# Kernel tuning notes

Hardware: AMD Instinct MI355X
Metric: run time of the kernel (lower is better)

## Reference

```python
import jax, jax.numpy as jnp
import numpy as np

DIM = 256
DEPTH = 6
HEADS = 8
DH = DIM // HEADS            # 32
BUCKET = 64
TEMP = 0.75                  # sort-net softmax temperature
FF = 4 * DIM
B, T = 4, 8192


def layernorm(x, g, b, eps=1e-5):
    m = x.mean(-1, keepdims=True)
    v = ((x - m) ** 2).mean(-1, keepdims=True)
    return (x - m) * jax.lax.rsqrt(v + eps) * g + b


def sinkhorn_attn(q, k, v):
    # q,k,v: (bh, t, dh). Bucketed attention with differentiable top-1 bucket routing
    bh, t, dh = q.shape
    nb = t // BUCKET
    bq = q.reshape(bh, nb, BUCKET, dh)
    bk = k.reshape(bh, nb, BUCKET, dh)
    bv = v.reshape(bh, nb, BUCKET, dh)
    # sort net: bucket summaries -> routing matrix R (differentiable_topk, k=1)
    sq = bq.mean(2)                                   # (bh, nb, dh)
    sk = bk.mean(2)
    R = jnp.einsum('bie,bje->bij', sq, sk) * (dh ** -0.5)
    probs = jax.nn.softmax(R / TEMP, axis=-1)
    top = jnp.max(probs, axis=-1, keepdims=True)      # (bh, nb, 1)
    idx = jnp.argmax(probs, axis=-1)                  # (bh, nb)
    Rtop = jax.nn.one_hot(idx, nb, dtype=q.dtype) * top
    # gather routed key/value buckets (weighted by routing prob)
    bk_r = jnp.einsum('bij,bjtd->bitd', Rtop, bk)
    bv_r = jnp.einsum('bij,bjtd->bitd', Rtop, bv)
    K = jnp.concatenate([bk_r, bk], axis=2)           # (bh, nb, 2*BUCKET, dh)
    V = jnp.concatenate([bv_r, bv], axis=2)
    dots = jnp.einsum('buie,buje->buij', bq, K) * (dh ** -0.5)
    attn = jax.nn.softmax(dots, axis=-1)
    out = jnp.einsum('buij,buje->buie', attn, V)
    return out.reshape(bh, t, dh)


def setup_inputs() -> dict:
    key = jax.random.key(0)
    ks = jax.random.split(key, 18)
    s = 0.02
    f32 = jnp.float32
    inp = {
        'x': jax.random.normal(ks[0], (B, DIM, T), f32),
        'pe0': jax.random.normal(ks[1], (T // BUCKET, DIM), f32) * s,
        'pe1': jax.random.normal(ks[2], (BUCKET, DIM), f32) * s,
        'ln1_g': jnp.ones((DEPTH, DIM), f32),
        'ln1_b': jnp.zeros((DEPTH, DIM), f32),
        'Wq': jax.random.normal(ks[3], (DEPTH, DIM, DIM), f32) * s,
        'Wkv': jax.random.normal(ks[4], (DEPTH, DIM, 2 * DIM), f32) * s,
        'Wo': jax.random.normal(ks[5], (DEPTH, DIM, DIM), f32) * s,
        'bo': jnp.zeros((DEPTH, DIM), f32),
        'ln2_g': jnp.ones((DEPTH, DIM), f32),
        'ln2_b': jnp.zeros((DEPTH, DIM), f32),
        'W1': jax.random.normal(ks[6], (DEPTH, DIM, FF), f32) * s,
        'b1': jnp.zeros((DEPTH, FF), f32),
        'W2': jax.random.normal(ks[7], (DEPTH, FF, DIM), f32) * s,
        'b2': jnp.zeros((DEPTH, DIM), f32),
        'gf': jnp.ones((DIM,), f32),
        'bf': jnp.zeros((DIM,), f32),
    }
    return inp


def _forward(x, pe0, pe1, ln1_g, ln1_b, Wq, Wkv, Wo, bo, ln2_g, ln2_b, W1, b1, W2, b2, gf, bf):
    b, _, t = x.shape
    y = jnp.transpose(x, (0, 2, 1))                      # (b, t, dim)
    pos = (pe0[:, None, :] + pe1[None, :, :]).reshape(-1, DIM)[:t]
    y = y + pos

    def split_heads(u):
        return u.reshape(b, t, HEADS, DH).transpose(0, 2, 1, 3).reshape(b * HEADS, t, DH)

    def step(y, p):
        g1, b1_, wq, wkv, wo, bo_, g2, b2_, w1, bb1, w2, bb2 = p
        h = layernorm(y, g1, b1_)
        q = h @ wq
        k, v = jnp.split(h @ wkv, 2, axis=-1)
        o = sinkhorn_attn(split_heads(q), split_heads(k), split_heads(v))
        o = o.reshape(b, HEADS, t, DH).transpose(0, 2, 1, 3).reshape(b, t, DIM)
        y = y + o @ wo + bo_
        h = layernorm(y, g2, b2_)
        y = y + jax.nn.gelu(h @ w1 + bb1, approximate=False) @ w2 + bb2
        return y, None

    y, _ = jax.lax.scan(step, y, (ln1_g, ln1_b, Wq, Wkv, Wo, bo, ln2_g, ln2_b, W1, b1, W2, b2))
    y = layernorm(y, gf, bf)
    return jnp.transpose(y, (0, 2, 1))


def reference(x, pe0, pe1, ln1_g, ln1_b, Wq, Wkv, Wo, bo, ln2_g, ln2_b, W1, b1, W2, b2, gf, bf):
    return _forward(x, pe0, pe1, ln1_g, ln1_b, Wq, Wkv, Wo, bo, ln2_g, ln2_b, W1, b1, W2, b2, gf, bf)
```

## Files before the change

### kernel.cpp

```cpp
#include <hip/hip_runtime.h>
#include <cstdint>
#include <cstddef>

#define T_LEN 8192
#define DIMC  256
#define NBUCK 128
#define BHEAD 32
#define MROWS 32768

typedef __attribute__((ext_vector_type(8))) short bf16x8;
typedef __attribute__((ext_vector_type(4))) float f32x4;

__device__ __forceinline__ ushort f2bf(float x) {
  union { float f; unsigned u; } v; v.f = x;
  unsigned r = v.u + 0x7fffu + ((v.u >> 16) & 1u);
  return (ushort)(r >> 16);
}
__device__ __forceinline__ float bf2f(ushort u) {
  union { unsigned u; float f; } v; v.u = ((unsigned)u) << 16; return v.f;
}

__device__ __forceinline__ void gld16(const void* g, void* l) {
  __builtin_amdgcn_global_load_lds((const __attribute__((address_space(1))) void*)g,
                                   (__attribute__((address_space(3))) void*)l, 16, 0, 0);
}

__device__ __forceinline__ float fast_gelu(float v) {
  float t2 = fmaf(v * v, 0.07135481283f, 1.5957691216f);
  float z  = v * t2;
  float e  = __expf(-z);
  return v * __builtin_amdgcn_rcpf(1.0f + e);
}

__global__ __launch_bounds__(256)
void add_pos_k(const float* __restrict__ x, const float* __restrict__ pe0,
               const float* __restrict__ pe1, float* __restrict__ y) {
  __shared__ float tile[32][33];
  int b  = blockIdx.z;
  int t0 = blockIdx.x * 32;
  int d0 = blockIdx.y * 32;
  int tj = threadIdx.x;
  int di = threadIdx.y;
#pragma unroll
  for (int k = 0; k < 4; k++) {
    int d = d0 + di + k * 8;
    tile[di + k * 8][tj] = x[((size_t)b * DIMC + d) * T_LEN + t0 + tj];
  }
  __syncthreads();
#pragma unroll
  for (int k = 0; k < 4; k++) {
    int t = t0 + di + k * 8;
    int d = d0 + tj;
    y[((size_t)b * T_LEN + t) * DIMC + d] =
        tile[tj][di + k * 8] + pe0[(size_t)(t >> 6) * DIMC + d] + pe1[(size_t)(t & 63) * DIMC + d];
  }
}

__global__ __launch_bounds__(256)
void layernorm_k(const float* __restrict__ x, const float* __restrict__ g,
                 const float* __restrict__ b, ushort* __restrict__ o) {
  int row  = blockIdx.x * 4 + (threadIdx.x >> 6);
  int lane = threadIdx.x & 63;
  const float4* xr = (const float4*)(x + (size_t)row * DIMC);
  float4 v = xr[lane];
  float s  = v.x + v.y + v.z + v.w;
  float s2 = v.x * v.x + v.y * v.y + v.z * v.z + v.w * v.w;
#pragma unroll
  for (int off = 32; off; off >>= 1) {
    s  += __shfl_xor(s, off);
    s2 += __shfl_xor(s2, off);
  }
  float mean = s * (1.0f / 256.0f);
  float var  = s2 * (1.0f / 256.0f) - mean * mean;
  float r    = rsqrtf(var + 1e-5f);
  float4 gv = ((const float4*)g)[lane];
  float4 bv = ((const float4*)b)[lane];
  ushort4 o4;
  o4.x = f2bf((v.x - mean) * r * gv.x + bv.x);
  o4.y = f2bf((v.y - mean) * r * gv.y + bv.y);
  o4.z = f2bf((v.z - mean) * r * gv.z + bv.z);
  o4.w = f2bf((v.w - mean) * r * gv.w + bv.w);
  ((ushort4*)(o + (size_t)row * DIMC))[lane] = o4;
}

__global__ __launch_bounds__(256)
void wt_bf16_k(const float* __restrict__ W, ushort* __restrict__ Wt,
               int K, int N, size_t outStride) {
  __shared__ float t[32][33];
  int l = blockIdx.z;
  const float* Wl = W + (size_t)l * K * N;
  ushort* Wtl = Wt + (size_t)l * outStride;
  int n0 = blockIdx.x * 32, k0 = blockIdx.y * 32;
  int tx = threadIdx.x, ty = threadIdx.y;
#pragma unroll
  for (int p = 0; p < 4; p++)
    t[ty + p * 8][tx] = Wl[(size_t)(k0 + ty + p * 8) * N + n0 + tx];
  __syncthreads();
#pragma unroll
  for (int p = 0; p < 4; p++)
    Wtl[(size_t)(n0 + ty + p * 8) * K + k0 + tx] = f2bf(t[tx][ty + p * 8]);
}

template <int EPI>
__global__ __launch_bounds__(256)
void gemm_bf16(const ushort* __restrict__ A, const ushort* __restrict__ Bt,
               const float* __restrict__ bias, ushort* __restrict__ Cbf,
               int N, int K, int lda, int ldb) {
  __shared__ ushort sm[2][8192];
  int tid = threadIdx.x;
  int w = tid >> 6, lane = tid & 63;
  int bm = blockIdx.x << 7, bn = blockIdx.y << 7;
  int wm = (w >> 1) << 6, wn = (w & 1) << 6;
  int l15 = lane & 15, quad = lane >> 4;

  int off0 = (w << 11) + (lane << 4);
  int r0 = off0 >> 6;
  int r1 = (off0 + 1024) >> 6;
  int swc = (((lane & 3) ^ ((lane >> 3) & 3)) << 3);
  const ushort* ga0 = A + (size_t)(bm + r0) * lda + swc;
  const ushort* ga1 = A + (size_t)(bm + r1) * lda + swc;
  const ushort* gb0 = Bt + (size_t)(bn + r0) * ldb + swc;
  const ushort* gb1 = Bt + (size_t)(bn + r1) * ldb + swc;
  int aoff0 = (w << 10);
  int aoff1 = aoff0 + 512;
  int boff0 = 4096 + (w << 10);
  int boff1 = boff0 + 512;

  int sq = quad ^ ((l15 >> 1) & 3);

  f32x4 acc[4][4];
#pragma unroll
  for (int i = 0; i < 4; i++)
#pragma unroll
    for (int j = 0; j < 4; j++) {
      f32x4 z = {0.f, 0.f, 0.f, 0.f};
      acc[i][j] = z;
    }

  gld16(ga0, &sm[0][aoff0]);
  gld16(ga1, &sm[0][aoff1]);
  gld16(gb0, &sm[0][boff0]);
  gld16(gb1, &sm[0][boff1]);
  __syncthreads();

  int cur = 0;
  for (int k0 = 0; k0 < K; k0 += 32) {
    if (k0 + 32 < K) {
      ushort* S = sm[cur ^ 1];
      gld16(ga0 + k0 + 32, S + aoff0);
      gld16(ga1 + k0 + 32, S + aoff1);
      gld16(gb0 + k0 + 32, S + boff0);
      gld16(gb1 + k0 + 32, S + boff1);
    }
    const ushort* Sc = sm[cur];
    bf16x8 aF[4], bF[4];
#pragma unroll
    for (int i = 0; i < 4; i++)
      aF[i] = *(const bf16x8*)(Sc + ((wm + (i << 4) + l15) << 5) + (sq << 3));
#pragma unroll
    for (int j = 0; j < 4; j++)
      bF[j] = *(const bf16x8*)(Sc + 4096 + ((wn + (j << 4) + l15) << 5) + (sq << 3));
#pragma unroll
    for (int i = 0; i < 4; i++)
#pragma unroll
      for (int j = 0; j < 4; j++)
        acc[i][j] = __builtin_amdgcn_mfma_f32_16x16x32_bf16(aF[i], bF[j], acc[i][j], 0, 0, 0);
    __syncthreads();
    cur ^= 1;
  }

  ushort (*eb)[16][66] = (ushort(*)[16][66])&sm[0][0];
  float bvj[4];
  if (EPI == 1) {
#pragma unroll
    for (int j = 0; j < 4; j++) bvj[j] = bias[bn + wn + (j << 4) + l15];
  }
#pragma unroll
  for (int i = 0; i < 4; i++) {
#pragma unroll
    for (int j = 0; j < 4; j++) {
#pragma unroll
      for (int r = 0; r < 4; r++) {
        float v = acc[i][j][r];
        if (EPI == 1) v = fast_gelu(v + bvj[j]);
        eb[w][(quad << 2) + r][(j << 4) + l15] = f2bf(v);
      }
    }
#pragma unroll
    for (int h = 0; h < 2; h++) {
      int chunk = (h << 6) + lane;
      int row = chunk >> 3, c8 = (chunk & 7) << 3;
      bf16x8 vv = *(const bf16x8*)&eb[w][row][c8];
      *(bf16x8*)&Cbf[(size_t)(bm + wm + (i << 4) + row) * N + bn + wn + c8] = vv;
    }
  }
}

template <int FINAL>
__global__ __launch_bounds__(512)
void oproj_ln_k(const ushort* __restrict__ A, const ushort* __restrict__ Bt,
                const float* __restrict__ bias, float* __restrict__ y,
                const float* __restrict__ g, const float* __restrict__ b,
                ushort* __restrict__ obf, int K, int lda) {
  __shared__ ushort smem[20480];
  int tid = threadIdx.x;
  int wid = tid >> 6, lane = tid & 63;
  int l15 = lane & 15, quad = lane >> 4;
  int bm = blockIdx.x << 6;
  int wm = (wid >> 2) << 5;
  int wn = (wid & 3) << 6;

  const ushort* gaB[2]; int lBoff[2];
#pragma unroll
  for (int p = 0; p < 2; p++) {
    int u = tid + (p << 9);
    int row = u >> 2, ch = u & 3;
    gaB[p] = Bt + (size_t)row * K + ((ch ^ ((row >> 1) & 3)) << 3);
    lBoff[p] = 2048 + (u << 3);
  }
  bool doA = (tid < 256);
  const ushort* gaA = A + (size_t)(bm + (tid >> 2)) * lda +
                      (((tid & 3) ^ ((tid >> 3) & 3)) << 3);
  int lAoff = tid << 3;

  int sq = quad ^ ((l15 >> 1) & 3);

  f32x4 acc[2][4];
#pragma unroll
  for (int i = 0; i < 2; i++)
#pragma unroll
    for (int j = 0; j < 4; j++) {
      f32x4 z = {0.f, 0.f, 0.f, 0.f};
      acc[i][j] = z;
    }

  if (doA) gld16(gaA, smem + lAoff);
#pragma unroll
  for (int p = 0; p < 2; p++) gld16(gaB[p], smem + lBoff[p]);
  __syncthreads();

  int cur = 0;
  for (int k0 = 0; k0 < K; k0 += 32) {
    if (k0 + 32 < K) {
      ushort* S = smem + ((cur ^ 1) ? 10240 : 0);
      if (doA) gld16(gaA + k0 + 32, S + lAoff);
#pragma unroll
      for (int p = 0; p < 2; p++) gld16(gaB[p] + k0 + 32, S + lBoff[p]);
    }
    const ushort* Sc = smem + (cur ? 10240 : 0);
    bf16x8 aF[2], bF[4];
#pragma unroll
    for (int i = 0; i < 2; i++)
      aF[i] = *(const bf16x8*)(Sc + ((wm + (i << 4) + l15) << 5) + (sq << 3));
#pragma unroll
    for (int j = 0; j < 4; j++)
      bF[j] = *(const bf16x8*)(Sc + 2048 + ((wn + (j << 4) + l15) << 5) + (sq << 3));
#pragma unroll
    for (int i = 0; i < 2; i++)
#pragma unroll
      for (int j = 0; j < 4; j++)
        acc[i][j] = __builtin_amdgcn_mfma_f32_16x16x32_bf16(aF[i], bF[j], acc[i][j], 0, 0, 0);
    __syncthreads();
    cur ^= 1;
  }

  float* vbuf = (float*)smem;
  float4 b4  = ((const float4*)bias)[lane];
  float4 g4  = ((const float4*)g)[lane];
  float4 bb4 = ((const float4*)b)[lane];
#pragma unroll
  for (int h = 0; h < 2; h++) {
    if ((wid >> 2) == h) {
#pragma unroll
      for (int i = 0; i < 2; i++)
#pragma unroll
        for (int j = 0; j < 4; j++)
#pragma unroll
          for (int r = 0; r < 4; r++)
            vbuf[((i << 4) + (quad << 2) + r) * 260 + wn + (j << 4) + l15] = acc[i][j][r];
    }
    __syncthreads();
#pragma unroll
    for (int rr = 0; rr < 4; rr++) {
      int lrow = (wid << 2) + rr;
      int row = bm + (h << 5) + lrow;
      float4 a4 = *(const float4*)&vbuf[lrow * 260 + (lane << 2)];
      const float4* yrow = (const float4*)&y[(size_t)row * 256];
      float4 y4 = yrow[lane];
      float4 v4;
      v4.x = a4.x + b4.x + y4.x;
      v4.y = a4.y + b4.y + y4.y;
      v4.z = a4.z + b4.z + y4.z;
      v4.w = a4.w + b4.w + y4.w;
      if (!FINAL) ((float4*)&y[(size_t)row * 256])[lane] = v4;
      float s1 = v4.x + v4.y + v4.z + v4.w;
      float s2 = v4.x * v4.x + v4.y * v4.y + v4.z * v4.z + v4.w * v4.w;
#pragma unroll
      for (int off = 32; off; off >>= 1) {
        s1 += __shfl_xor(s1, off);
        s2 += __shfl_xor(s2, off);
      }
      float mean = s1 * (1.0f / 256.0f);
      float var  = s2 * (1.0f / 256.0f) - mean * mean;
      float rstd = rsqrtf(var + 1e-5f);
      float4 o4;
      o4.x = (v4.x - mean) * rstd * g4.x + bb4.x;
      o4.y = (v4.y - mean) * rstd * g4.y + bb4.y;
      o4.z = (v4.z - mean) * rstd * g4.z + bb4.z;
      o4.w = (v4.w - mean) * rstd * g4.w + bb4.w;
      if (FINAL) {
        ((float4*)&y[(size_t)row * 256])[lane] = o4;
      } else {
        ushort4 u4;
        u4.x = f2bf(o4.x); u4.y = f2bf(o4.y); u4.z = f2bf(o4.z); u4.w = f2bf(o4.w);
        ((ushort4*)&obf[(size_t)row * 256])[lane] = u4;
      }
    }
    __syncthreads();
  }
}

__global__ __launch_bounds__(64)
void summary_k(const ushort* __restrict__ qkv,
               float* __restrict__ sq, float* __restrict__ sk) {
  int blk = blockIdx.x;
  int bh = blk >> 7, ib = blk & 127;
  int b = bh >> 3, h = bh & 7;
  int lane = threadIdx.x;
  int d = lane & 31;
  bool isK = lane >= 32;
  size_t base = ((size_t)b * T_LEN + (size_t)ib * 64) * 768 + (isK ? 256 : 0) + h * 32 + d;
  float s = 0.f;
#pragma unroll 8
  for (int t = 0; t < 64; t++) s += bf2f(qkv[base + (size_t)t * 768]);
  s *= (1.0f / 64.0f);
  float* dst = isK ? sk : sq;
  dst[((size_t)bh * NBUCK + ib) * 32 + d] = s;
}

__global__ __launch_bounds__(64)
void route_k(const float* __restrict__ sq, const float* __restrict__ sk,
             int* __restrict__ ridx, float* __restrict__ rw) {
  int blk = blockIdx.x;
  int bh = blk >> 7, ib = blk & 127;
  int lane = threadIdx.x;
  const float* qrow = sq + ((size_t)bh * NBUCK + ib) * 32;
  const float* k0 = sk + ((size_t)bh * NBUCK + lane) * 32;
  const float* k1 = k0 + 64 * 32;
  float s0 = 0.f, s1 = 0.f;
#pragma unroll
  for (int d = 0; d < 32; d++) {
    float qd = qrow[d];
    s0 += qd * k0[d];
    s1 += qd * k1[d];
  }
  const float sc = 0.17677669529663687f * (4.0f / 3.0f);
  float L0 = s0 * sc, L1 = s1 * sc;
  float m = fmaxf(L0, L1);
#pragma unroll
  for (int off = 32; off; off >>= 1) m = fmaxf(m, __shfl_xor(m, off));
  float Z = expf(L0 - m) + expf(L1 - m);
#pragma unroll
  for (int off = 32; off; off >>= 1) Z += __shfl_xor(Z, off);
  float mv = (L1 > L0) ? L1 : L0;
  int mj = (L1 > L0) ? lane + 64 : lane;
#pragma unroll
  for (int off = 32; off; off >>= 1) {
    float ov = __shfl_xor(mv, off);
    int oj = __shfl_xor(mj, off);
    if (ov > mv || (ov == mv && oj < mj)) { mv = ov; mj = oj; }
  }
  if (lane == 0) {
    ridx[blk] = mj;
    rw[blk] = 1.0f / Z;
  }
}

__global__ __launch_bounds__(256)
void attn_mfma_k(const ushort* __restrict__ qkv,
                 const int* __restrict__ ridx, const float* __restrict__ rw,
                 ushort* __restrict__ o) {
  __shared__ ushort Qs[64][40];
  __shared__ ushort Ks[128][40];
  __shared__ ushort Vt[32][136];
  __shared__ ushort Ps[4][16][136];
  int blk = blockIdx.x;
  int bh = blk >> 7, ib = blk & 127;
  int b = bh >> 3, h = bh & 7;
  int tid = threadIdx.x;
  int jr = ridx[blk];
  float w = rw[blk];
  {
    int r = tid >> 2, c = (tid & 3) << 3;
    const ushort* src = qkv + ((size_t)b * T_LEN + (size_t)ib * 64 + r) * 768 + h * 32 + c;
    *(bf16x8*)&Qs[r][c] = *(const bf16x8*)src;
  }
#pragma unroll
  for (int p = 0; p < 2; p++) {
    int idx = tid + (p << 8);
    int r = idx >> 2, c = (idx & 3) << 3;
    int srcb = (r < 64) ? jr : ib;
    int tt = r & 63;
    const ushort* src = qkv + ((size_t)b * T_LEN + (size_t)srcb * 64 + tt) * 768 + 256 + h * 32 + c;
    *(bf16x8*)&Ks[r][c] = *(const bf16x8*)src;
  }
  {
    int tok = tid >> 1, d0 = (tid & 1) << 4;
    int srcb = (tok < 64) ? jr : ib;
    int tt = tok & 63;
    const ushort* src = qkv + ((size_t)b * T_LEN + (size_t)srcb * 64 + tt) * 768 + 512 + h * 32 + d0;
    bf16x8 v0 = *(const bf16x8*)src;
    bf16x8 v1 = *(const bf16x8*)(src + 8);
#pragma unroll
    for (int j = 0; j < 8; j++) {
      Vt[d0 + j][tok] = (ushort)v0[j];
      Vt[d0 + 8 + j][tok] = (ushort)v1[j];
    }
  }
  __syncthreads();
  int wid = tid >> 6, lane = tid & 63, l15 = lane & 15, quad = lane >> 4;
  bf16x8 aQ = *(const bf16x8*)&Qs[(wid << 4) + l15][quad << 3];
  f32x4 sf[8];
#pragma unroll
  for (int jn = 0; jn < 8; jn++) {
    bf16x8 bK = *(const bf16x8*)&Ks[(jn << 4) + l15][quad << 3];
    f32x4 z = {0.f, 0.f, 0.f, 0.f};
    sf[jn] = __builtin_amdgcn_mfma_f32_16x16x32_bf16(aQ, bK, z, 0, 0, 0);
  }
  const float sc = 0.17677669529663687f;
#pragma unroll
  for (int jn = 0; jn < 8; jn++) {
    float mult = (jn < 4) ? w * sc : sc;
#pragma unroll
    for (int r = 0; r < 4; r++) sf[jn][r] *= mult;
  }
  float mx[4], sm[4], inv[4];
#pragma unroll
  for (int r = 0; r < 4; r++) {
    float m = sf[0][r];
#pragma unroll
    for (int jn = 1; jn < 8; jn++) m = fmaxf(m, sf[jn][r]);
    mx[r] = m;
  }
#pragma unroll
  for (int off = 1; off < 16; off <<= 1)
#pragma unroll
    for (int r = 0; r < 4; r++) mx[r] = fmaxf(mx[r], __shfl_xor(mx[r], off));
#pragma unroll
  for (int r = 0; r < 4; r++) sm[r] = 0.f;
#pragma unroll
  for (int jn = 0; jn < 8; jn++)
#pragma unroll
    for (int r = 0; r < 4; r++) {
      sf[jn][r] = __expf(sf[jn][r] - mx[r]);
      sm[r] += sf[jn][r];
    }
#pragma unroll
  for (int off = 1; off < 16; off <<= 1)
#pragma unroll
    for (int r = 0; r < 4; r++) sm[r] += __shfl_xor(sm[r], off);
#pragma unroll
  for (int r = 0; r < 4; r++) inv[r] = __builtin_amdgcn_rcpf(sm[r]);
#pragma unroll
  for (int jn = 0; jn < 8; jn++) {
    float ws2 = (jn < 4) ? w : 1.f;
#pragma unroll
    for (int r = 0; r < 4; r++)
      Ps[wid][(quad << 2) + r][(jn << 4) + l15] = f2bf(sf[jn][r] * inv[r] * ws2);
  }
  f32x4 of[2];
#pragma unroll
  for (int nd = 0; nd < 2; nd++) { f32x4 z = {0.f, 0.f, 0.f, 0.f}; of[nd] = z; }
#pragma unroll
  for (int kk = 0; kk < 4; kk++) {
    bf16x8 aP = *(const bf16x8*)&Ps[wid][l15][(kk << 5) + (quad << 3)];
#pragma unroll
    for (int nd = 0; nd < 2; nd++) {
      bf16x8 bV = *(const bf16x8*)&Vt[(nd << 4) + l15][(kk << 5) + (quad << 3)];
      of[nd] = __builtin_amdgcn_mfma_f32_16x16x32_bf16(aP, bV, of[nd], 0, 0, 0);
    }
  }
  ushort* obase = o + ((size_t)b * T_LEN + (size_t)ib * 64 + (wid << 4) + (quad << 2)) * 256 + h * 32 + l15;
#pragma unroll
  for (int nd = 0; nd < 2; nd++)
#pragma unroll
    for (int r = 0; r < 4; r++)
      obase[(size_t)r * 256 + (nd << 4)] = f2bf(of[nd][r]);
}

__global__ __launch_bounds__(256)
void transpose_out_k(const float* __restrict__ yln, float* __restrict__ out) {
  __shared__ float tile[32][33];
  int b  = blockIdx.z;
  int t0 = blockIdx.x * 32;
  int d0 = blockIdx.y * 32;
  int tx = threadIdx.x;
  int ty = threadIdx.y;
#pragma unroll
  for (int k = 0; k < 4; k++) {
    int t = t0 + ty + k * 8;
    tile[ty + k * 8][tx] = yln[((size_t)b * T_LEN + t) * DIMC + d0 + tx];
  }
  __syncthreads();
#pragma unroll
  for (int k = 0; k < 4; k++) {
    int d = d0 + ty + k * 8;
    out[((size_t)b * DIMC + d) * T_LEN + t0 + tx] = tile[tx][ty + k * 8];
  }
}

extern "C" void kernel_launch(void* const* d_in, const int* in_sizes, int n_in,
                              void* d_out, int out_size, void* d_ws, size_t ws_size,
                              hipStream_t stream) {
  const float* x     = (const float*)d_in[0];
  const float* pe0   = (const float*)d_in[1];
  const float* pe1   = (const float*)d_in[2];
  const float* ln1_g = (const float*)d_in[3];
  const float* ln1_b = (const float*)d_in[4];
  const float* Wq    = (const float*)d_in[5];
  const float* Wkv   = (const float*)d_in[6];
  const float* Wo    = (const float*)d_in[7];
  const float* bo    = (const float*)d_in[8];
  const float* ln2_g = (const float*)d_in[9];
  const float* ln2_b = (const float*)d_in[10];
  const float* W1    = (const float*)d_in[11];
  const float* b1    = (const float*)d_in[12];
  const float* W2    = (const float*)d_in[13];
  const float* b2    = (const float*)d_in[14];
  const float* gf    = (const float*)d_in[15];
  const float* bfp   = (const float*)d_in[16];
  float* out = (float*)d_out;

  const int M = MROWS;
  float*  y    = (float*)d_ws;
  ushort* qkv  = (ushort*)(y + (size_t)M * 256);
  ushort* bufA = qkv + (size_t)M * 768;
  ushort* bufB = bufA + (size_t)M * 256;
  ushort* wbf  = bufB + (size_t)M * 256;
  float*  sqb  = (float*)(wbf + (size_t)6 * 786432);
  float*  skb  = sqb + 131072;
  float*  rwb  = skb + 131072;
  int*    rib  = (int*)(rwb + 4096);
  ushort* ffbf = qkv;

  dim3 tb(32, 8);
  wt_bf16_k<<<dim3(8, 8, 6),  tb, 0, stream>>>(Wq,  wbf + 0,      256, 256,  786432);
  wt_bf16_k<<<dim3(16, 8, 6), tb, 0, stream>>>(Wkv, wbf + 65536,  256, 512,  786432);
  wt_bf16_k<<<dim3(8, 8, 6),  tb, 0, stream>>>(Wo,  wbf + 196608, 256, 256,  786432);
  wt_bf16_k<<<dim3(32, 8, 6), tb, 0, stream>>>(W1,  wbf + 262144, 256, 1024, 786432);
  wt_bf16_k<<<dim3(8, 32, 6), tb, 0, stream>>>(W2,  wbf + 524288, 1024, 256, 786432);

  add_pos_k<<<dim3(T_LEN / 32, DIMC / 32, 4), tb, 0, stream>>>(x, pe0, pe1, y);
  layernorm_k<<<M / 4, 256, 0, stream>>>(y, ln1_g, ln1_b, bufB);

  for (int l = 0; l < 6; l++) {
    const ushort* wl    = wbf + (size_t)l * 786432;
    const ushort* wqkvT = wl;
    const ushort* woT   = wl + 196608;
    const ushort* w1T   = wl + 262144;
    const ushort* w2T   = wl + 524288;

    gemm_bf16<0><<<dim3(M / 128, 6), 256, 0, stream>>>(bufB, wqkvT, nullptr, qkv, 768, 256, 256, 256);
    summary_k<<<BHEAD * NBUCK, 64, 0, stream>>>(qkv, sqb, skb);
    route_k<<<BHEAD * NBUCK, 64, 0, stream>>>(sqb, skb, rib, rwb);
    attn_mfma_k<<<BHEAD * NBUCK, 256, 0, stream>>>(qkv, rib, rwb, bufA);
    oproj_ln_k<0><<<M / 64, 512, 0, stream>>>(bufA, woT, bo + l * 256, y,
                                              ln2_g + l * 256, ln2_b + l * 256,
                                              bufB, 256, 256);
    gemm_bf16<1><<<dim3(M / 128, 8), 256, 0, stream>>>(bufB, w1T, b1 + l * 1024, ffbf, 1024, 256, 256, 256);
    if (l < 5) {
      oproj_ln_k<0><<<M / 64, 512, 0, stream>>>(ffbf, w2T, b2 + l * 256, y,
                                                ln1_g + (l + 1) * 256, ln1_b + (l + 1) * 256,
                                                bufB, 1024, 1024);
    } else {
      oproj_ln_k<1><<<M / 64, 512, 0, stream>>>(ffbf, w2T, b2 + l * 256, y,
                                                gf, bfp, nullptr, 1024, 1024);
    }
  }

  transpose_out_k<<<dim3(T_LEN / 32, DIMC / 32, 4), tb, 0, stream>>>(y, out);

  (void)in_sizes; (void)n_in; (void)out_size; (void)ws_size;
}
```

Baseline: 1.151 ms.

## Give each wave private LDS tiles and drop block barriers in GEMM loops

Both GEMM kernels now have each wave stage its own A and B sub-tiles into a private LDS region, so the main k-loop synchronises with a per-wave waitcnt fence instead of a block-wide __syncthreads. The o-proj+LayerNorm kernel shrinks to 32 rows per block with 256 threads, and its epilogue collapses to a single vbuf pass. The aim is to remove block-level barrier stalls. In exchange, shared A/B data is loaded redundantly by several waves, which raises global/L2 traffic and LDS footprint, and the full vmcnt(0) wait removes overlap of the next-tile prefetch with compute.

Result: slower. 1.342 ms (+16.6%).

```diff
diff --git a/kernel.cpp b/kernel.cpp
--- a/kernel.cpp
+++ b/kernel.cpp
@@ -24,6 +24,11 @@
   __builtin_amdgcn_global_load_lds((const __attribute__((address_space(1))) void*)g,
                                    (__attribute__((address_space(3))) void*)l, 16, 0, 0);
 }
+
+#define WAVE_FENCE do { \
+    asm volatile("s_waitcnt vmcnt(0) lgkmcnt(0)" ::: "memory"); \
+    __builtin_amdgcn_sched_barrier(0); \
+  } while (0)
 
 __device__ __forceinline__ float fast_gelu(float v) {
   float t2 = fmaf(v * v, 0.07135481283f, 1.5957691216f);
@@ -106,26 +111,26 @@
 void gemm_bf16(const ushort* __restrict__ A, const ushort* __restrict__ Bt,
                const float* __restrict__ bias, ushort* __restrict__ Cbf,
                int N, int K, int lda, int ldb) {
-  __shared__ ushort sm[2][8192];
+  __shared__ ushort sm[32768];
   int tid = threadIdx.x;
   int w = tid >> 6, lane = tid & 63;
   int bm = blockIdx.x << 7, bn = blockIdx.y << 7;
   int wm = (w >> 1) << 6, wn = (w & 1) << 6;
   int l15 = lane & 15, quad = lane >> 4;
-
-  int off0 = (w << 11) + (lane << 4);
-  int r0 = off0 >> 6;
-  int r1 = (off0 + 1024) >> 6;
-  int swc = (((lane & 3) ^ ((lane >> 3) & 3)) << 3);
-  const ushort* ga0 = A + (size_t)(bm + r0) * lda + swc;
-  const ushort* ga1 = A + (size_t)(bm + r1) * lda + swc;
-  const ushort* gb0 = Bt + (size_t)(bn + r0) * ldb + swc;
-  const ushort* gb1 = Bt + (size_t)(bn + r1) * ldb + swc;
-  int aoff0 = (w << 10);
-  int aoff1 = aoff0 + 512;
-  int boff0 = 4096 + (w << 10);
-  int boff1 = boff0 + 512;
-
+  int wreg = w << 13;
+
+  const ushort* gA[4]; int lA[4];
+  const ushort* gB[4]; int lB[4];
+#pragma unroll
+  for (int p = 0; p < 4; p++) {
+    int s = (p << 6) + lane;
+    int row = s >> 2, ch = s & 3;
+    int swz = ((ch ^ ((row >> 1) & 3)) << 3);
+    gA[p] = A + (size_t)(bm + wm + row) * lda + swz;
+    gB[p] = Bt + (size_t)(bn + wn + row) * ldb + swz;
+    lA[p] = (s << 3);
+    lB[p] = 2048 + (s << 3);
+  }
   int sq = quad ^ ((l15 >> 1) & 3);
 
   f32x4 acc[4][4];
@@ -137,39 +142,45 @@
       acc[i][j] = z;
     }
 
-  gld16(ga0, &sm[0][aoff0]);
-  gld16(ga1, &sm[0][aoff1]);
-  gld16(gb0, &sm[0][boff0]);
-  gld16(gb1, &sm[0][boff1]);
-  __syncthreads();
+  const int T = K >> 5;
+#pragma unroll
+  for (int p = 0; p < 4; p++) gld16(gA[p], sm + wreg + lA[p]);
+#pragma unroll
+  for (int p = 0; p < 4; p++) gld16(gB[p], sm + wreg + lB[p]);
+  WAVE_FENCE;
 
   int cur = 0;
-  for (int k0 = 0; k0 < K; k0 += 32) {
-    if (k0 + 32 < K) {
-      ushort* S = sm[cur ^ 1];
-      gld16(ga0 + k0 + 32, S + aoff0);
-      gld16(ga1 + k0 + 32, S + aoff1);
-      gld16(gb0 + k0 + 32, S + boff0);
-      gld16(gb1 + k0 + 32, S + boff1);
-    }
-    const ushort* Sc = sm[cur];
+  for (int t = 0; t < T; t++) {
+    if (t + 1 < T) {
+      ushort* S = sm + wreg + ((cur ^ 1) ? 4096 : 0);
+      int kn = (t + 1) << 5;
+#pragma unroll
+      for (int p = 0; p < 4; p++) gld16(gA[p] + kn, S + lA[p]);
+#pragma unroll
+      for (int p = 0; p < 4; p++) gld16(gB[p] + kn, S + lB[p]);
+    }
+    const ushort* Sc = sm + wreg + (cur ? 4096 : 0);
     bf16x8 aF[4], bF[4];
 #pragma unroll
-    for (int i = 0; i < 4; i++)
-      aF[i] = *(const bf16x8*)(Sc + ((wm + (i << 4) + l15) << 5) + (sq << 3));
-#pragma unroll
-    for (int j = 0; j < 4; j++)
-      bF[j] = *(const bf16x8*)(Sc + 4096 + ((wn + (j << 4) + l15) << 5) + (sq << 3));
+    for (int i = 0; i < 4; i++) {
+      int row = (i << 4) + l15;
+      aF[i] = *(const bf16x8*)(Sc + (((row << 2) + sq) << 3));
+    }
+#pragma unroll
+    for (int j = 0; j < 4; j++) {
+      int row = (j << 4) + l15;
+      bF[j] = *(const bf16x8*)(Sc + 2048 + (((row << 2) + sq) << 3));
+    }
 #pragma unroll
     for (int i = 0; i < 4; i++)
 #pragma unroll
       for (int j = 0; j < 4; j++)
         acc[i][j] = __builtin_amdgcn_mfma_f32_16x16x32_bf16(aF[i], bF[j], acc[i][j], 0, 0, 0);
-    __syncthreads();
+    WAVE_FENCE;
     cur ^= 1;
   }
 
-  ushort (*eb)[16][66] = (ushort(*)[16][66])&sm[0][0];
+  ushort (*ebw)[66] = (ushort(*)[66])(sm + wreg);
   float bvj[4];
   if (EPI == 1) {
 #pragma unroll
@@ -183,46 +194,49 @@
       for (int r = 0; r < 4; r++) {
         float v = acc[i][j][r];
         if (EPI == 1) v = fast_gelu(v + bvj[j]);
-        eb[w][(quad << 2) + r][(j << 4) + l15] = f2bf(v);
+        ebw[(quad << 2) + r][(j << 4) + l15] = f2bf(v);
       }
     }
 #pragma unroll
     for (int h = 0; h < 2; h++) {
       int chunk = (h << 6) + lane;
       int row = chunk >> 3, c8 = (chunk & 7) << 3;
-      bf16x8 vv = *(const bf16x8*)&eb[w][row][c8];
+      bf16x8 vv = *(const bf16x8*)&ebw[row][c8];
       *(bf16x8*)&Cbf[(size_t)(bm + wm + (i << 4) + row) * N + bn + wn + c8] = vv;
     }
   }
 }
 
 template <int FINAL>
-__global__ __launch_bounds__(512)
+__global__ __launch_bounds__(256)
 void oproj_ln_k(const ushort* __restrict__ A, const ushort* __restrict__ Bt,
                 const float* __restrict__ bias, float* __restrict__ y,
                 const float* __restrict__ g, const float* __restrict__ b,
                 ushort* __restrict__ obf, int K, int lda) {
-  __shared__ ushort smem[20480];
+  __shared__ ushort smem[24576];
   int tid = threadIdx.x;
   int wid = tid >> 6, lane = tid & 63;
   int l15 = lane & 15, quad = lane >> 4;
-  int bm = blockIdx.x << 6;
-  int wm = (wid >> 2) << 5;
-  int wn = (wid & 3) << 6;
-
-  const ushort* gaB[2]; int lBoff[2];
+  int bm = blockIdx.x << 5;
+  int wn = wid << 6;
+  int wreg = wid * 6144;
+
+  const ushort* gA[2]; int lA[2];
 #pragma unroll
   for (int p = 0; p < 2; p++) {
-    int u = tid + (p << 9);
-    int row = u >> 2, ch = u & 3;
-    gaB[p] = Bt + (size_t)row * K + ((ch ^ ((row >> 1) & 3)) << 3);
-    lBoff[p] = 2048 + (u << 3);
-  }
-  bool doA = (tid < 256);
-  const ushort* gaA = A + (size_t)(bm + (tid >> 2)) * lda +
-                      (((tid & 3) ^ ((tid >> 3) & 3)) << 3);
-  int lAoff = tid << 3;
-
+    int s = (p << 6) + lane;
+    int row = s >> 2, ch = s & 3;
+    gA[p] = A + (size_t)(bm + row) * lda + ((ch ^ ((row >> 1) & 3)) << 3);
+    lA[p] = (s << 3);
+  }
+  const ushort* gB[4]; int lB[4];
+#pragma unroll
+  for (int p = 0; p < 4; p++) {
+    int s = (p << 6) + lane;
+    int row = s >> 2, ch = s & 3;
+    gB[p] = Bt + (size_t)(wn + row) * K + ((ch ^ ((row >> 1) & 3)) << 3);
+    lB[p] = 1024 + (s << 3);
+  }
   int sq = quad ^ ((l15 >> 1) & 3);
 
   f32x4 acc[2][4];
@@ -234,89 +248,91 @@
       acc[i][j] = z;
     }
 
-  if (doA) gld16(gaA, smem + lAoff);
-#pragma unroll
-  for (int p = 0; p < 2; p++) gld16(gaB[p], smem + lBoff[p]);
-  __syncthreads();
+  const int T = K >> 5;
+#pragma unroll
+  for (int p = 0; p < 2; p++) gld16(gA[p], smem + wreg + lA[p]);
+#pragma unroll
+  for (int p = 0; p < 4; p++) gld16(gB[p], smem + wreg + lB[p]);
+  WAVE_FENCE;
 
   int cur = 0;
-  for (int k0 = 0; k0 < K; k0 += 32) {
-    if (k0 + 32 < K) {
-      ushort* S = smem + ((cur ^ 1) ? 10240 : 0);
-      if (doA) gld16(gaA + k0 + 32, S + lAoff);
-#pragma unroll
-      for (int p = 0; p < 2; p++) gld16(gaB[p] + k0 + 32, S + lBoff[p]);
-    }
-    const ushort* Sc = smem + (cur ? 10240 : 0);
+  for (int t = 0; t < T; t++) {
+    if (t + 1 < T) {
+      ushort* S = smem + wreg + ((cur ^ 1) ? 3072 : 0);
+      int kn = (t + 1) << 5;
+#pragma unroll
+      for (int p = 0; p < 2; p++) gld16(gA[p] + kn, S + lA[p]);
+#pragma unroll
+      for (int p = 0; p < 4; p++) gld16(gB[p] + kn, S + lB[p]);
+    }
+    const ushort* Sc = smem + wreg + (cur ? 3072 : 0);
     bf16x8 aF[2], bF[4];
 #pragma unroll
-    for (int i = 0; i < 2; i++)
-      aF[i] = *(const bf16x8*)(Sc + ((wm + (i << 4) + l15) << 5) + (sq << 3));
-#pragma unroll
-    for (int j = 0; j < 4; j++)
-      bF[j] = *(const bf16x8*)(Sc + 2048 + ((wn + (j << 4) + l15) << 5) + (sq << 3));
+    for (int i = 0; i < 2; i++) {
+      int row = (i << 4) + l15;
+      aF[i] = *(const bf16x8*)(Sc + (((row << 2) + sq) << 3));
+    }
+#pragma unroll
+    for (int j = 0; j < 4; j++) {
+      int row = (j << 4) + l15;
+      bF[j] = *(const bf16x8*)(Sc + 1024 + (((row << 2) + sq) << 3));
+    }
 #pragma unroll
     for (int i = 0; i < 2; i++)
 #pragma unroll
       for (int j = 0; j < 4; j++)
         acc[i][j] = __builtin_amdgcn_mfma_f32_16x16x32_bf16(aF[i], bF[j], acc[i][j], 0, 0, 0);
-    __syncthreads();
+    WAVE_FENCE;
     cur ^= 1;
   }
 
+  __syncthreads();
   float* vbuf = (float*)smem;
+#pragma unroll
+  for (int i = 0; i < 2; i++)
+#pragma unroll
+    for (int j = 0; j < 4; j++)
+#pragma unroll
+      for (int r = 0; r < 4; r++)
+        vbuf[((i << 4) + (quad << 2) + r) * 260 + wn + (j << 4) + l15] = acc[i][j][r];
+  __syncthreads();
   float4 b4  = ((const float4*)bias)[lane];
   float4 g4  = ((const float4*)g)[lane];
   float4 bb4 = ((const float4*)b)[lane];
 #pragma unroll
-  for (int h = 0; h < 2; h++) {
-    if ((wid >> 2) == h) {
-#pragma unroll
-      for (int i = 0; i < 2; i++)
-#pragma unroll
-        for (int j = 0; j < 4; j++)
-#pragma unroll
-          for (int r = 0; r < 4; r++)
-            vbuf[((i << 4) + (quad << 2) + r) * 260 + wn + (j << 4) + l15] = acc[i][j][r];
-    }
-    __syncthreads();
-#pragma unroll
-    for (int rr = 0; rr < 4; rr++) {
-      int lrow = (wid << 2) + rr;
-      int row = bm + (h << 5) + lrow;
-      float4 a4 = *(const float4*)&vbuf[lrow * 260 + (lane << 2)];
-      const float4* yrow = (const float4*)&y[(size_t)row * 256];
-      float4 y4 = yrow[lane];
-      float4 v4;
-      v4.x = a4.x + b4.x + y4.x;
-      v4.y = a4.y + b4.y + y4.y;
-      v4.z = a4.z + b4.z + y4.z;
-      v4.w = a4.w + b4.w + y4.w;
-      if (!FINAL) ((float4*)&y[(size_t)row * 256])[lane] = v4;
-      float s1 = v4.x + v4.y + v4.z + v4.w;
-      float s2 = v4.x * v4.x + v4.y * v4.y + v4.z * v4.z + v4.w * v4.w;
-#pragma unroll
-      for (int off = 32; off; off >>= 1) {
-        s1 += __shfl_xor(s1, off);
-        s2 += __shfl_xor(s2, off);
-      }
-      float mean = s1 * (1.0f / 256.0f);
-      float var  = s2 * (1.0f / 256.0f) - mean * mean;
-      float rstd = rsqrtf(var + 1e-5f);
-      float4 o4;
-      o4.x = (v4.x - mean) * rstd * g4.x + bb4.x;
-      o4.y = (v4.y - mean) * rstd * g4.y + bb4.y;
-      o4.z = (v4.z - mean) * rstd * g4.z + bb4.z;
-      o4.w = (v4.w - mean) * rstd * g4.w + bb4.w;
-      if (FINAL) {
-        ((float4*)&y[(size_t)row * 256])[lane] = o4;
-      } else {
-        ushort4 u4;
-        u4.x = f2bf(o4.x); u4.y = f2bf(o4.y); u4.z = f2bf(o4.z); u4.w = f2bf(o4.w);
-        ((ushort4*)&obf[(size_t)row * 256])[lane] = u4;
-      }
-    }
-    __syncthreads();
+  for (int rr = 0; rr < 8; rr++) {
+    int lrow = (wid << 3) + rr;
+    int row = bm + lrow;
+    float4 a4 = *(const float4*)&vbuf[lrow * 260 + (lane << 2)];
+    float4 y4 = ((const float4*)&y[(size_t)row * 256])[lane];
+    float4 v4;
+    v4.x = a4.x + b4.x + y4.x;
+    v4.y = a4.y + b4.y + y4.y;
+    v4.z = a4.z + b4.z + y4.z;
+    v4.w = a4.w + b4.w + y4.w;
+    if (!FINAL) ((float4*)&y[(size_t)row * 256])[lane] = v4;
+    float s1 = v4.x + v4.y + v4.z + v4.w;
+    float s2 = v4.x * v4.x + v4.y * v4.y + v4.z * v4.z + v4.w * v4.w;
+#pragma unroll
+    for (int off = 32; off; off >>= 1) {
+      s1 += __shfl_xor(s1, off);
+      s2 += __shfl_xor(s2, off);
+    }
+    float mean = s1 * (1.0f / 256.0f);
+    float var  = s2 * (1.0f / 256.0f) - mean * mean;
+    float rstd = rsqrtf(var + 1e-5f);
+    float4 o4;
+    o4.x = (v4.x - mean) * rstd * g4.x + bb4.x;
+    o4.y = (v4.y - mean) * rstd * g4.y + bb4.y;
+    o4.z = (v4.z - mean) * rstd * g4.z + bb4.z;
+    o4.w = (v4.w - mean) * rstd * g4.w + bb4.w;
+    if (FINAL) {
+      ((float4*)&y[(size_t)row * 256])[lane] = o4;
+    } else {
+      ushort4 u4;
+      u4.x = f2bf(o4.x); u4.y = f2bf(o4.y); u4.z = f2bf(o4.z); u4.w = f2bf(o4.w);
+      ((ushort4*)&obf[(size_t)row * 256])[lane] = u4;
+    }
   }
 }
 
@@ -564,16 +580,16 @@
     summary_k<<<BHEAD * NBUCK, 64, 0, stream>>>(qkv, sqb, skb);
     route_k<<<BHEAD * NBUCK, 64, 0, stream>>>(sqb, skb, rib, rwb);
     attn_mfma_k<<<BHEAD * NBUCK, 256, 0, stream>>>(qkv, rib, rwb, bufA);
-    oproj_ln_k<0><<<M / 64, 512, 0, stream>>>(bufA, woT, bo + l * 256, y,
+    oproj_ln_k<0><<<M / 32, 256, 0, stream>>>(bufA, woT, bo + l * 256, y,
                                               ln2_g + l * 256, ln2_b + l * 256,
                                               bufB, 256, 256);
     gemm_bf16<1><<<dim3(M / 128, 8), 256, 0, stream>>>(bufB, w1T, b1 + l * 1024, ffbf, 1024, 256, 256, 256);
     if (l < 5) {
-      oproj_ln_k<0><<<M / 64, 512, 0, stream>>>(ffbf, w2T, b2 + l * 256, y,
+      oproj_ln_k<0><<<M / 32, 256, 0, stream>>>(ffbf, w2T, b2 + l * 256, y,
                                                 ln1_g + (l + 1) * 256, ln1_b + (l + 1) * 256,
                                                 bufB, 1024, 1024);
     } else {
-      oproj_ln_k<1><<<M / 64, 512, 0, stream>>>(ffbf, w2T, b2 + l * 256, y,
+      oproj_ln_k<1><<<M / 32, 256, 0, stream>>>(ffbf, w2T, b2 + l * 256, y,
                                                 gf, bfp, nullptr, 1024, 1024);
     }
   }
```
